# Optimization experiments

Hardware: AMD Instinct MI355X
Metric: run time of the kernel (lower is better)

## Reference

```python
import jax, jax.numpy as jnp
import numpy as np

T, D, H = 1024, 256, 256


def mish(x):
    return x * jnp.tanh(jax.nn.softplus(x))


def layer_norm(x, w, b, eps=1e-5):
    mu = x.mean(-1, keepdims=True)
    var = ((x - mu) ** 2).mean(-1, keepdims=True)
    return (x - mu) / jnp.sqrt(var + eps) * w + b


def setup_inputs() -> dict:
    key = jax.random.key(0)
    ks = jax.random.split(key, 12)
    def glorot(k, sh, fan_in):
        return (jax.random.normal(k, sh, jnp.float32) / np.sqrt(fan_in)).astype(jnp.float32)
    return {
        "x": jax.random.normal(ks[0], (T, D), jnp.float32),
        "s0": jnp.zeros((1, H, H), jnp.float32),
        "z0": jnp.zeros((1, H), jnp.float32),
        "start": jax.random.randint(ks[1], (T + 1,), 0, 2, jnp.int32),
        "done": jax.random.randint(ks[2], (T + 1,), 0, 2, jnp.int32),
        "Wk": glorot(ks[3], (H, D), D),
        "Wq": glorot(ks[4], (H, D), D),
        "Wv": glorot(ks[5], (H, D), D),
        "Wskip": glorot(ks[6], (H, D), D),
        "bskip": jnp.zeros((H,), jnp.float32),
        "W1": glorot(ks[7], (H, H), H),
        "b1": jnp.zeros((H,), jnp.float32),
        "W2": glorot(ks[8], (H, H), H),
        "b2": jnp.zeros((H,), jnp.float32),
        "W3": glorot(ks[9], (H, H), H),
        "b3": jnp.zeros((H,), jnp.float32),
        "ln_w": jnp.ones((H,), jnp.float32),
        "ln_b": jnp.zeros((H,), jnp.float32),
    }


def reference(x, s0, z0, start, done, Wk, Wq, Wv, Wskip, bskip, W1, b1, W2, b2, W3, b3, ln_w, ln_b):
    # feature maps (equinox Linear: y = W @ x, weight is (out,in))
    k = jax.nn.elu(x @ Wk.T)          # [T,H]
    q = jax.nn.elu(x @ Wq.T)          # [T,H]
    v = x @ Wv.T                      # [T,H]
    st = start.astype(x.dtype)[:, None]   # [T+1,1] reset-continuation flags
    dn = done.astype(x.dtype)[:, None]    # [T+1,1]
    # prepend carried state to the sequence, as in the original
    kv = jnp.concatenate([s0, jnp.einsum('ti,tj->tij', k, v)], axis=0)  # [T+1,H,H]
    kk = jnp.concatenate([z0, k], axis=0)                               # [T+1,H]
    def combine(a, b):
        s_a, z_a, _, _ = a
        kv_b, k_b, st_b, dn_b = b
        s = s_a * st_b[..., None] + kv_b * dn_b[..., None]
        z = z_a * st_b + k_b * dn_b
        return (s, z, st_b, dn_b)
    s, z, _, _ = jax.lax.associative_scan(combine, (kv, kk, st, dn))
    # drop the initial-state slot so time indices align with queries
    s_t, z_t = s[1:], z[1:]                          # [T,H,H], [T,H]
    numer = jnp.einsum('ti,tij->tj', q, s_t)         # [T,H]
    denom = jnp.einsum('ti,tj->t', z_t, q).clip(1e-5)  # faithful to source einsum
    out = numer / denom[:, None]
    h = mish(out @ W1.T + b1)
    h = mish(h @ W2.T + b2)
    h = h @ W3.T + b3
    return layer_norm(h + (x @ Wskip.T + bskip), ln_w, ln_b)
```

## Files before the change

kernel.cpp:

```cpp
#include <hip/hip_runtime.h>
#include <math.h>


typedef unsigned long long u64;
typedef unsigned short u16;
typedef __attribute__((ext_vector_type(8))) unsigned short us8;
typedef __attribute__((ext_vector_type(4))) unsigned short us4;
typedef __attribute__((ext_vector_type(8))) short s8;
typedef __attribute__((ext_vector_type(4))) float f4;

__device__ __forceinline__ float eluf(float v) { return v > 0.f ? v : expm1f(v); }
__device__ __forceinline__ float mishf(float v) {
  float sp = fmaxf(v, 0.f) + log1pf(expf(-fabsf(v)));
  return v * tanhf(sp);
}
__device__ __forceinline__ u16 f2bf(float f) {
  unsigned u = __float_as_uint(f);
  unsigned r = u + 0x7FFFu + ((u >> 16) & 1u);
  return (u16)(r >> 16);
}
__device__ __forceinline__ float bf2f(u16 h) { return __uint_as_float((unsigned)h << 16); }

__device__ __forceinline__ f4 mfma16(const u16* a, const u16* b, f4 c) {
  s8 av = *(const s8*)(const void*)a;
  s8 bv = *(const s8*)(const void*)b;
  return __builtin_amdgcn_mfma_f32_16x16x32_bf16(av, bv, c, 0, 0, 0);
}

__device__ __forceinline__ u64 expand32(u64 x) {
  x &= 0xFFFFFFFFull;
  x = (x | (x << 16)) & 0x0000FFFF0000FFFFull;
  x = (x | (x << 8))  & 0x00FF00FF00FF00FFull;
  x = (x | (x << 4))  & 0x0F0F0F0F0F0F0F0Full;
  x = (x | (x << 2))  & 0x3333333333333333ull;
  x = (x | (x << 1))  & 0x5555555555555555ull;
  return x | (x << 1);
}

__device__ __forceinline__ us8 cvt8(const float* p) {
  float4 a = *(const float4*)p;
  float4 b = *(const float4*)(p + 4);
  us8 v;
  v[0] = f2bf(a.x); v[1] = f2bf(a.y); v[2] = f2bf(a.z); v[3] = f2bf(a.w);
  v[4] = f2bf(b.x); v[5] = f2bf(b.y); v[6] = f2bf(b.z); v[7] = f2bf(b.w);
  return v;
}

__global__ __launch_bounds__(256) void qkvs_mask(const float* __restrict__ x,
    const float* __restrict__ Wk, const float* __restrict__ Wq,
    const float* __restrict__ Wv, const float* __restrict__ Wsk,
    const float* __restrict__ bskip,
    const int* __restrict__ start, const int* __restrict__ done,
    u16* __restrict__ Kb, u16* __restrict__ Qb, u16* __restrict__ Vb,
    float* __restrict__ SKP, float* __restrict__ Kpart, u64* __restrict__ Mb) {
  __shared__ u64 SMEM[5810];
  const int tid = threadIdx.x;
  if (blockIdx.x < 256) {
    u16* Xs = (u16*)SMEM;
    u16* Ws = Xs + 2560;
    const int wave = tid >> 6, l = tid & 63;
    const int l15 = l & 15, quad = l >> 4;
    const int rt = blockIdx.x & 15, my = blockIdx.x >> 4;
    const int mat = my >> 2, nt = my & 3;
    const int n0 = nt * 64, mbase = rt * 64;
    const float* Wsrc = (mat == 0) ? Wk : (mat == 1) ? Wq : (mat == 2) ? Wv : Wsk;
    f4 acc[4];
#pragma unroll
    for (int s = 0; s < 4; s++) acc[s] = (f4){0.f, 0.f, 0.f, 0.f};
    const int srow = tid >> 2, sko = (tid & 3) * 8;
    for (int kt = 0; kt < 8; kt++) {
      *(us8*)&Xs[srow * 40 + sko] = cvt8(&x[(mbase + srow) * 256 + kt * 32 + sko]);
      *(us8*)&Ws[srow * 40 + sko] = cvt8(&Wsrc[(n0 + srow) * 256 + kt * 32 + sko]);
      __syncthreads();
      const u16* ap = &Xs[(wave * 16 + l15) * 40 + quad * 8];
#pragma unroll
      for (int s = 0; s < 4; s++)
        acc[s] = mfma16(ap, &Ws[(s * 16 + l15) * 40 + quad * 8], acc[s]);
      __syncthreads();
    }
    const int mw = mbase + wave * 16 + quad * 4;
    if (mat == 0) {
      float tmp[4][4];
#pragma unroll
      for (int s = 0; s < 4; s++)
#pragma unroll
        for (int r = 0; r < 4; r++) {
          float v = eluf(acc[s][r]);
          tmp[s][r] = v;
          Kb[(mw + r) * 256 + n0 + s * 16 + l15] = f2bf(v);
        }
#pragma unroll
      for (int r = 0; r < 4; r++) {
        float t = tmp[0][r] + tmp[1][r] + tmp[2][r] + tmp[3][r];
#pragma unroll
        for (int off = 1; off <= 8; off <<= 1) t += __shfl_xor(t, off);
        if (l15 == 0) Kpart[nt * 1024 + mw + r] = t;
      }
    } else if (mat == 1) {
#pragma unroll
      for (int s = 0; s < 4; s++)
#pragma unroll
        for (int r = 0; r < 4; r++)
          Qb[(mw + r) * 256 + n0 + s * 16 + l15] = f2bf(eluf(acc[s][r]));
    } else if (mat == 2) {
#pragma unroll
      for (int s = 0; s < 4; s++)
#pragma unroll
        for (int r = 0; r < 4; r++)
          Vb[(mw + r) * 256 + n0 + s * 16 + l15] = f2bf(acc[s][r]);
    } else {
#pragma unroll
      for (int s = 0; s < 4; s++) {
        int n = n0 + s * 16 + l15;
        float bv = bskip[n];
#pragma unroll
        for (int r = 0; r < 4; r++)
          SKP[(mw + r) * 256 + n] = acc[s][r] + bv;
      }
    }
    return;
  }
  u64* LV = SMEM;
  unsigned char* sB = (unsigned char*)(SMEM + 5540);
  unsigned char* dB = sB + 1028;
  for (int i = tid; i < 1025; i += 256) {
    sB[i] = (unsigned char)(start[i] != 0);
    dB[i] = (unsigned char)(done[i] != 0);
  }
  if (tid == 0) LV[0] = 1ull;
  __syncthreads();
  const int LOFF[11] = {0, 1407, 383, 127, 63, 31, 15, 7, 3, 1, 0};
  const int GOFF[10] = {5503, 5520, 5528, 5532, 5534, 5535, 5536, 5537, 5538, 5539};
  if (tid < 37) {
    int lv, w;
    if (tid < 17)      { lv = 0; w = tid; }
    else if (tid < 25) { lv = 1; w = tid - 17; }
    else if (tid < 29) { lv = 2; w = tid - 25; }
    else if (tid < 31) { lv = 3; w = tid - 29; }
    else               { lv = tid - 27; w = 0; }
    int n = 1024 >> lv;
    u64 g = 0;
    for (int b = 0; b < 64; b++) {
      int j = (w << 6) + b;
      if (j >= n) break;
      unsigned char bit = (j & 1) ? dB[((j + 1) << lv) - 1] : sB[((j + 2) << lv) - 1];
      g |= (u64)bit << b;
    }
    LV[GOFF[lv] + w] = g;
  }
  __syncthreads();
#pragma unroll
  for (int lv = 9; lv >= 1; lv--) {
    const int n = 1024 >> lv;
    const int nw = (n >= 64) ? (n >> 6) : 1;
    const int nwp = (n >= 128) ? (n >> 7) : 1;
    const int total = n * nw;
    for (int idx = tid; idx < total; idx += 256) {
      int t = idx / nw, w = idx - t * nw;
      u64 word;
      if (t == 0) word = (w == 0) ? 1ull : 0ull;
      else {
        int p = (t & 1) ? (t >> 1) : (t >> 1) - 1;
        u64 pw = LV[LOFF[lv + 1] + p * nwp + (w >> 1)];
        u64 e = expand32((w & 1) ? (pw >> 32) : pw) & LV[GOFF[lv] + w];
        if (t & 1) word = e;
        else {
          int gi = ((t + 1) << lv) - 1;
          word = sB[gi] ? e : 0ull;
          if ((t >> 6) == w) word |= (u64)dB[gi] << (t & 63);
        }
      }
      LV[LOFF[lv] + t * nw + w] = word;
    }
    __syncthreads();
  }
  for (int idx = tid; idx < 1024 * 16; idx += 256) {
    int tp = idx >> 4, wp = idx & 15;
    int t = tp + 1;
    int p = (t & 1) ? (t >> 1) : (t >> 1) - 1;
    u64 sw[2];
#pragma unroll
    for (int u = 0; u < 2; u++) {
      int w = wp + u;
      u64 e = 0;
      if (w < 16) {
        u64 pw = LV[1407 + p * 8 + (w >> 1)];
        e = expand32((w & 1) ? (pw >> 32) : pw) & LV[GOFF[0] + w];
      }
      if (t & 1) sw[u] = e;
      else {
        u64 word = sB[t] ? e : 0ull;
        if ((t >> 6) == w) word |= (u64)dB[t] << (t & 63);
        sw[u] = word;
      }
    }
    Mb[tp * 16 + wp] = (sw[0] >> 1) | (sw[1] << 63);
  }
}

__global__ __launch_bounds__(512) void attn_mlp(
    const u16* __restrict__ Kb, const u16* __restrict__ Qb, const u16* __restrict__ Vb,
    const float* __restrict__ Kpart, const float* __restrict__ SKP,
    const u64* __restrict__ Mb,
    const float* __restrict__ W1, const float* __restrict__ W2, const float* __restrict__ W3,
    const float* __restrict__ b1, const float* __restrict__ b2, const float* __restrict__ b3,
    const float* __restrict__ lnw, const float* __restrict__ lnb,
    float* __restrict__ outp) {
  __shared__ float Ks[1024];
  __shared__ u64 Mw[64];
  __shared__ u16 As[16 * 264];
  __shared__ float Op[8][256];
  __shared__ float dp[8];
  __shared__ u16 WsAll[8 * 640];
  __shared__ float Hbuf[4 * 260];
  const int tid = threadIdx.x, wave = tid >> 6, l = tid & 63;
  const int l15 = l & 15, quad = l >> 4;
  const int m0 = blockIdx.x * 4;
  {
    int j = tid * 2;
    Ks[j] = Kpart[j] + Kpart[1024 + j] + Kpart[2048 + j] + Kpart[3072 + j];
    Ks[j + 1] = Kpart[j + 1] + Kpart[1024 + j + 1] + Kpart[2048 + j + 1] + Kpart[3072 + j + 1];
    if (tid < 64) Mw[tid] = Mb[(m0 + (tid >> 4)) * 16 + (tid & 15)];
  }
  __syncthreads();
  const int r = wave & 3, h = wave >> 2;
  const int tp = m0 + r;
  float q[4], O[4] = {0.f, 0.f, 0.f, 0.f};
  {
    us4 qv = *(const us4*)&Qb[tp * 256 + l * 4];
    q[0] = bf2f(qv.x); q[1] = bf2f(qv.y); q[2] = bf2f(qv.z); q[3] = bf2f(qv.w);
  }
  float qs = q[0] + q[1] + q[2] + q[3];
#pragma unroll
  for (int off = 1; off <= 32; off <<= 1) qs += __shfl_xor(qs, off);
  float d = 0.f;
  for (int w = h * 8; w < h * 8 + 8; w++) {
    u64 bits = Mw[r * 16 + w];
    while (bits) {
      int b = __builtin_ctzll(bits);
      bits &= bits - 1;
      int j = w * 64 + b;
      us4 kv = *(const us4*)&Kb[j * 256 + l * 4];
      us4 vv = *(const us4*)&Vb[j * 256 + l * 4];
      float s = q[0] * bf2f(kv.x) + q[1] * bf2f(kv.y) + q[2] * bf2f(kv.z) + q[3] * bf2f(kv.w);
#pragma unroll
      for (int off = 1; off <= 32; off <<= 1) s += __shfl_xor(s, off);
      d += Ks[j];
      O[0] += s * bf2f(vv.x); O[1] += s * bf2f(vv.y);
      O[2] += s * bf2f(vv.z); O[3] += s * bf2f(vv.w);
    }
  }
#pragma unroll
  for (int i = 0; i < 4; i++) Op[wave][l * 4 + i] = O[i];
  if (l == 0) dp[wave] = d;
  __syncthreads();
  if (h == 0) {
    float dd = dp[r] + dp[r + 4];
    float inv = 1.f / fmaxf(qs * dd, 1e-5f);
    us4 o;
    o.x = f2bf((O[0] + Op[r + 4][l * 4 + 0]) * inv);
    o.y = f2bf((O[1] + Op[r + 4][l * 4 + 1]) * inv);
    o.z = f2bf((O[2] + Op[r + 4][l * 4 + 2]) * inv);
    o.w = f2bf((O[3] + Op[r + 4][l * 4 + 3]) * inv);
    *(us4*)&As[r * 264 + l * 4] = o;
  }
  __syncthreads();
  u16* Wsw = WsAll + wave * 640;
  const int wr = l >> 2, wko = (l & 3) * 8;
#pragma unroll 1
  for (int layer = 0; layer < 3; layer++) {
    const float* Wl = (layer == 0) ? W1 : (layer == 1) ? W2 : W3;
    const float* bias = (layer == 0) ? b1 : (layer == 1) ? b2 : b3;
    f4 acc[2];
#pragma unroll
    for (int c = 0; c < 2; c++) {
      const int nt = wave * 2 + c;
      acc[c] = (f4){0.f, 0.f, 0.f, 0.f};
      for (int kt = 0; kt < 8; kt++) {
        *(us8*)&Wsw[wr * 40 + wko] = cvt8(&Wl[(nt * 16 + wr) * 256 + kt * 32 + wko]);
        const u16* ap = &As[l15 * 264 + kt * 32 + quad * 8];
        acc[c] = mfma16(ap, &Wsw[l15 * 40 + quad * 8], acc[c]);
      }
    }
    __syncthreads();
    if (quad == 0) {
#pragma unroll
      for (int c = 0; c < 2; c++) {
        const int n = (wave * 2 + c) * 16 + l15;
        float bv = bias[n];
        if (layer < 2) {
#pragma unroll
          for (int rr = 0; rr < 4; rr++)
            As[rr * 264 + n] = f2bf(mishf(acc[c][rr] + bv));
        } else {
#pragma unroll
          for (int rr = 0; rr < 4; rr++)
            Hbuf[rr * 260 + n] = acc[c][rr] + bv + SKP[(m0 + rr) * 256 + n];
        }
      }
    }
    __syncthreads();
  }
  if (wave < 4) {
    float hv[4];
#pragma unroll
    for (int i = 0; i < 4; i++) hv[i] = Hbuf[wave * 260 + l * 4 + i];
    float s1 = hv[0] + hv[1] + hv[2] + hv[3];
    float s2 = hv[0] * hv[0] + hv[1] * hv[1] + hv[2] * hv[2] + hv[3] * hv[3];
#pragma unroll
    for (int off = 1; off <= 32; off <<= 1) {
      s1 += __shfl_xor(s1, off);
      s2 += __shfl_xor(s2, off);
    }
    float mu = s1 * (1.f / 256.f);
    float var = s2 * (1.f / 256.f) - mu * mu;
    float rs = rsqrtf(fmaxf(var, 0.f) + 1e-5f);
    float4 wv = *(const float4*)&lnw[l * 4];
    float4 bv = *(const float4*)&lnb[l * 4];
    float4 o;
    o.x = (hv[0] - mu) * rs * wv.x + bv.x;
    o.y = (hv[1] - mu) * rs * wv.y + bv.y;
    o.z = (hv[2] - mu) * rs * wv.z + bv.z;
    o.w = (hv[3] - mu) * rs * wv.w + bv.w;
    *(float4*)&outp[(m0 + wave) * 256 + l * 4] = o;
  }
}

extern "C" void kernel_launch(void* const* d_in, const int* in_sizes, int n_in,
                              void* d_out, int out_size, void* d_ws, size_t ws_size,
                              hipStream_t stream) {
  (void)in_sizes; (void)n_in; (void)out_size; (void)ws_size;
  const float* x   = (const float*)d_in[0];
  const int* start = (const int*)d_in[3];
  const int* done  = (const int*)d_in[4];
  const float* Wk  = (const float*)d_in[5];
  const float* Wq  = (const float*)d_in[6];
  const float* Wv  = (const float*)d_in[7];
  const float* Wsk = (const float*)d_in[8];
  const float* bsk = (const float*)d_in[9];
  const float* W1  = (const float*)d_in[10];
  const float* b1  = (const float*)d_in[11];
  const float* W2  = (const float*)d_in[12];
  const float* b2  = (const float*)d_in[13];
  const float* W3  = (const float*)d_in[14];
  const float* b3  = (const float*)d_in[15];
  const float* lnw = (const float*)d_in[16];
  const float* lnb = (const float*)d_in[17];
  float* out = (float*)d_out;

  char* w = (char*)d_ws;
  u16* Kb      = (u16*)w;
  u16* Qb      = (u16*)(w + 524288);
  u16* Vb      = (u16*)(w + 1048576);
  float* SKP   = (float*)(w + 1572864);
  float* Kpart = (float*)(w + 2621440);
  u64* Mb      = (u64*)(w + 2637824);

  qkvs_mask<<<257, 256, 0, stream>>>(x, Wk, Wq, Wv, Wsk, bsk, start, done,
                                     Kb, Qb, Vb, SKP, Kpart, Mb);
  attn_mlp<<<256, 512, 0, stream>>>(Kb, Qb, Vb, Kpart, SKP, Mb,
                                    W1, W2, W3, b1, b2, b3, lnw, lnb, out);
}
```

Measured before the change: 159.5 us.

## Compute per-block reset mask chain in attention kernel instead of serial mask block

Removes the single serial mask-building block from the projection kernel. Each attention block now rebuilds only the mask path for its own four query rows from start/done flags, using wave ballots for the group words. This takes a long single-block tree over all timesteps off the critical path. In exchange every attention block redoes some flag loading and nine small synchronized levels.

Result: faster. 133.5 us (-16.3%).

```diff
diff --git a/kernel.cpp b/kernel.cpp
--- a/kernel.cpp
+++ b/kernel.cpp
@@ -46,167 +46,87 @@
   return v;
 }
 
-__global__ __launch_bounds__(256) void qkvs_mask(const float* __restrict__ x,
+__global__ __launch_bounds__(256) void qkvs_mfma(const float* __restrict__ x,
     const float* __restrict__ Wk, const float* __restrict__ Wq,
     const float* __restrict__ Wv, const float* __restrict__ Wsk,
     const float* __restrict__ bskip,
-    const int* __restrict__ start, const int* __restrict__ done,
     u16* __restrict__ Kb, u16* __restrict__ Qb, u16* __restrict__ Vb,
-    float* __restrict__ SKP, float* __restrict__ Kpart, u64* __restrict__ Mb) {
-  __shared__ u64 SMEM[5810];
-  const int tid = threadIdx.x;
-  if (blockIdx.x < 256) {
-    u16* Xs = (u16*)SMEM;
-    u16* Ws = Xs + 2560;
-    const int wave = tid >> 6, l = tid & 63;
-    const int l15 = l & 15, quad = l >> 4;
-    const int rt = blockIdx.x & 15, my = blockIdx.x >> 4;
-    const int mat = my >> 2, nt = my & 3;
-    const int n0 = nt * 64, mbase = rt * 64;
-    const float* Wsrc = (mat == 0) ? Wk : (mat == 1) ? Wq : (mat == 2) ? Wv : Wsk;
-    f4 acc[4];
-#pragma unroll
-    for (int s = 0; s < 4; s++) acc[s] = (f4){0.f, 0.f, 0.f, 0.f};
-    const int srow = tid >> 2, sko = (tid & 3) * 8;
-    for (int kt = 0; kt < 8; kt++) {
-      *(us8*)&Xs[srow * 40 + sko] = cvt8(&x[(mbase + srow) * 256 + kt * 32 + sko]);
-      *(us8*)&Ws[srow * 40 + sko] = cvt8(&Wsrc[(n0 + srow) * 256 + kt * 32 + sko]);
-      __syncthreads();
-      const u16* ap = &Xs[(wave * 16 + l15) * 40 + quad * 8];
-#pragma unroll
-      for (int s = 0; s < 4; s++)
-        acc[s] = mfma16(ap, &Ws[(s * 16 + l15) * 40 + quad * 8], acc[s]);
-      __syncthreads();
-    }
-    const int mw = mbase + wave * 16 + quad * 4;
-    if (mat == 0) {
-      float tmp[4][4];
-#pragma unroll
-      for (int s = 0; s < 4; s++)
-#pragma unroll
-        for (int r = 0; r < 4; r++) {
-          float v = eluf(acc[s][r]);
-          tmp[s][r] = v;
-          Kb[(mw + r) * 256 + n0 + s * 16 + l15] = f2bf(v);
-        }
+    float* __restrict__ SKP, float* __restrict__ Kpart) {
+  __shared__ u16 Xs[64 * 40], Ws[64 * 40];
+  const int tid = threadIdx.x, wave = tid >> 6, l = tid & 63;
+  const int l15 = l & 15, quad = l >> 4;
+  const int rt = blockIdx.x & 15, my = blockIdx.x >> 4;
+  const int mat = my >> 2, nt = my & 3;
+  const int n0 = nt * 64, mbase = rt * 64;
+  const float* Wsrc = (mat == 0) ? Wk : (mat == 1) ? Wq : (mat == 2) ? Wv : Wsk;
+  f4 acc[4];
+#pragma unroll
+  for (int s = 0; s < 4; s++) acc[s] = (f4){0.f, 0.f, 0.f, 0.f};
+  const int srow = tid >> 2, sko = (tid & 3) * 8;
+  for (int kt = 0; kt < 8; kt++) {
+    *(us8*)&Xs[srow * 40 + sko] = cvt8(&x[(mbase + srow) * 256 + kt * 32 + sko]);
+    *(us8*)&Ws[srow * 40 + sko] = cvt8(&Wsrc[(n0 + srow) * 256 + kt * 32 + sko]);
+    __syncthreads();
+    const u16* ap = &Xs[(wave * 16 + l15) * 40 + quad * 8];
+#pragma unroll
+    for (int s = 0; s < 4; s++)
+      acc[s] = mfma16(ap, &Ws[(s * 16 + l15) * 40 + quad * 8], acc[s]);
+    __syncthreads();
+  }
+  const int mw = mbase + wave * 16 + quad * 4;
+  if (mat == 0) {
+    float tmp[4][4];
+#pragma unroll
+    for (int s = 0; s < 4; s++)
 #pragma unroll
       for (int r = 0; r < 4; r++) {
-        float t = tmp[0][r] + tmp[1][r] + tmp[2][r] + tmp[3][r];
-#pragma unroll
-        for (int off = 1; off <= 8; off <<= 1) t += __shfl_xor(t, off);
-        if (l15 == 0) Kpart[nt * 1024 + mw + r] = t;
-      }
-    } else if (mat == 1) {
-#pragma unroll
-      for (int s = 0; s < 4; s++)
-#pragma unroll
-        for (int r = 0; r < 4; r++)
-          Qb[(mw + r) * 256 + n0 + s * 16 + l15] = f2bf(eluf(acc[s][r]));
-    } else if (mat == 2) {
-#pragma unroll
-      for (int s = 0; s < 4; s++)
-#pragma unroll
-        for (int r = 0; r < 4; r++)
-          Vb[(mw + r) * 256 + n0 + s * 16 + l15] = f2bf(acc[s][r]);
-    } else {
-#pragma unroll
-      for (int s = 0; s < 4; s++) {
-        int n = n0 + s * 16 + l15;
-        float bv = bskip[n];
-#pragma unroll
-        for (int r = 0; r < 4; r++)
-          SKP[(mw + r) * 256 + n] = acc[s][r] + bv;
-      }
-    }
-    return;
-  }
-  u64* LV = SMEM;
-  unsigned char* sB = (unsigned char*)(SMEM + 5540);
-  unsigned char* dB = sB + 1028;
-  for (int i = tid; i < 1025; i += 256) {
-    sB[i] = (unsigned char)(start[i] != 0);
-    dB[i] = (unsigned char)(done[i] != 0);
-  }
-  if (tid == 0) LV[0] = 1ull;
-  __syncthreads();
-  const int LOFF[11] = {0, 1407, 383, 127, 63, 31, 15, 7, 3, 1, 0};
-  const int GOFF[10] = {5503, 5520, 5528, 5532, 5534, 5535, 5536, 5537, 5538, 5539};
-  if (tid < 37) {
-    int lv, w;
-    if (tid < 17)      { lv = 0; w = tid; }
-    else if (tid < 25) { lv = 1; w = tid - 17; }
-    else if (tid < 29) { lv = 2; w = tid - 25; }
-    else if (tid < 31) { lv = 3; w = tid - 29; }
-    else               { lv = tid - 27; w = 0; }
-    int n = 1024 >> lv;
-    u64 g = 0;
-    for (int b = 0; b < 64; b++) {
-      int j = (w << 6) + b;
-      if (j >= n) break;
-      unsigned char bit = (j & 1) ? dB[((j + 1) << lv) - 1] : sB[((j + 2) << lv) - 1];
-      g |= (u64)bit << b;
-    }
-    LV[GOFF[lv] + w] = g;
-  }
-  __syncthreads();
-#pragma unroll
-  for (int lv = 9; lv >= 1; lv--) {
-    const int n = 1024 >> lv;
-    const int nw = (n >= 64) ? (n >> 6) : 1;
-    const int nwp = (n >= 128) ? (n >> 7) : 1;
-    const int total = n * nw;
-    for (int idx = tid; idx < total; idx += 256) {
-      int t = idx / nw, w = idx - t * nw;
-      u64 word;
-      if (t == 0) word = (w == 0) ? 1ull : 0ull;
-      else {
-        int p = (t & 1) ? (t >> 1) : (t >> 1) - 1;
-        u64 pw = LV[LOFF[lv + 1] + p * nwp + (w >> 1)];
-        u64 e = expand32((w & 1) ? (pw >> 32) : pw) & LV[GOFF[lv] + w];
-        if (t & 1) word = e;
-        else {
-          int gi = ((t + 1) << lv) - 1;
-          word = sB[gi] ? e : 0ull;
-          if ((t >> 6) == w) word |= (u64)dB[gi] << (t & 63);
-        }
-      }
-      LV[LOFF[lv] + t * nw + w] = word;
-    }
-    __syncthreads();
-  }
-  for (int idx = tid; idx < 1024 * 16; idx += 256) {
-    int tp = idx >> 4, wp = idx & 15;
-    int t = tp + 1;
-    int p = (t & 1) ? (t >> 1) : (t >> 1) - 1;
-    u64 sw[2];
-#pragma unroll
-    for (int u = 0; u < 2; u++) {
-      int w = wp + u;
-      u64 e = 0;
-      if (w < 16) {
-        u64 pw = LV[1407 + p * 8 + (w >> 1)];
-        e = expand32((w & 1) ? (pw >> 32) : pw) & LV[GOFF[0] + w];
-      }
-      if (t & 1) sw[u] = e;
-      else {
-        u64 word = sB[t] ? e : 0ull;
-        if ((t >> 6) == w) word |= (u64)dB[t] << (t & 63);
-        sw[u] = word;
-      }
-    }
-    Mb[tp * 16 + wp] = (sw[0] >> 1) | (sw[1] << 63);
+        float v = eluf(acc[s][r]);
+        tmp[s][r] = v;
+        Kb[(mw + r) * 256 + n0 + s * 16 + l15] = f2bf(v);
+      }
+#pragma unroll
+    for (int r = 0; r < 4; r++) {
+      float t = tmp[0][r] + tmp[1][r] + tmp[2][r] + tmp[3][r];
+#pragma unroll
+      for (int off = 1; off <= 8; off <<= 1) t += __shfl_xor(t, off);
+      if (l15 == 0) Kpart[nt * 1024 + mw + r] = t;
+    }
+  } else if (mat == 1) {
+#pragma unroll
+    for (int s = 0; s < 4; s++)
+#pragma unroll
+      for (int r = 0; r < 4; r++)
+        Qb[(mw + r) * 256 + n0 + s * 16 + l15] = f2bf(eluf(acc[s][r]));
+  } else if (mat == 2) {
+#pragma unroll
+    for (int s = 0; s < 4; s++)
+#pragma unroll
+      for (int r = 0; r < 4; r++)
+        Vb[(mw + r) * 256 + n0 + s * 16 + l15] = f2bf(acc[s][r]);
+  } else {
+#pragma unroll
+    for (int s = 0; s < 4; s++) {
+      int n = n0 + s * 16 + l15;
+      float bv = bskip[n];
+#pragma unroll
+      for (int r = 0; r < 4; r++)
+        SKP[(mw + r) * 256 + n] = acc[s][r] + bv;
+    }
   }
 }
 
 __global__ __launch_bounds__(512) void attn_mlp(
     const u16* __restrict__ Kb, const u16* __restrict__ Qb, const u16* __restrict__ Vb,
     const float* __restrict__ Kpart, const float* __restrict__ SKP,
-    const u64* __restrict__ Mb,
+    const int* __restrict__ start, const int* __restrict__ done,
     const float* __restrict__ W1, const float* __restrict__ W2, const float* __restrict__ W3,
     const float* __restrict__ b1, const float* __restrict__ b2, const float* __restrict__ b3,
     const float* __restrict__ lnw, const float* __restrict__ lnb,
     float* __restrict__ outp) {
   __shared__ float Ks[1024];
+  __shared__ unsigned char sBs[1028], dBs[1028];
+  __shared__ u64 GS[37];
+  __shared__ u64 CH[4][21];
   __shared__ u64 Mw[64];
   __shared__ u16 As[16 * 264];
   __shared__ float Op[8][256];
@@ -216,11 +136,80 @@
   const int tid = threadIdx.x, wave = tid >> 6, l = tid & 63;
   const int l15 = l & 15, quad = l >> 4;
   const int m0 = blockIdx.x * 4;
+  for (int i = tid; i < 1025; i += 512) {
+    sBs[i] = (unsigned char)(start[i] != 0);
+    dBs[i] = (unsigned char)(done[i] != 0);
+  }
   {
     int j = tid * 2;
     Ks[j] = Kpart[j] + Kpart[1024 + j] + Kpart[2048 + j] + Kpart[3072 + j];
     Ks[j + 1] = Kpart[j + 1] + Kpart[1024 + j + 1] + Kpart[2048 + j + 1] + Kpart[3072 + j + 1];
-    if (tid < 64) Mw[tid] = Mb[(m0 + (tid >> 4)) * 16 + (tid & 15)];
+  }
+  if (wave < 4 && l == 0) CH[wave][20] = 1ull;
+  __syncthreads();
+  if (wave >= 4) {
+    for (int job = wave - 4; job < 37; job += 4) {
+      int lv, w;
+      if (job < 17)      { lv = 0; w = job; }
+      else if (job < 25) { lv = 1; w = job - 17; }
+      else if (job < 29) { lv = 2; w = job - 25; }
+      else if (job < 31) { lv = 3; w = job - 29; }
+      else               { lv = job - 27; w = 0; }
+      int n = 1024 >> lv;
+      int j = w * 64 + l;
+      int ok = 0;
+      if (j < n)
+        ok = (j & 1) ? dBs[((j + 1) << lv) - 1] : sBs[((j + 2) << lv) - 1];
+      u64 word = __ballot(ok != 0);
+      if (l == 0) GS[(lv == 0) ? w : (lv == 1) ? 17 + w : (lv == 2) ? 25 + w
+                     : (lv == 3) ? 29 + w : 27 + lv] = word;
+    }
+  }
+  __syncthreads();
+  const int CHOFF[11] = {0, 0, 8, 12, 14, 15, 16, 17, 18, 19, 20};
+  const int GOFF2[10] = {0, 17, 25, 29, 31, 32, 33, 34, 35, 36};
+#pragma unroll 1
+  for (int lv = 9; lv >= 1; lv--) {
+    if (wave < 4) {
+      int nw = (1024 >> lv) >= 64 ? ((1024 >> lv) >> 6) : 1;
+      if (l < nw) {
+        int rr = m0 + wave + 1;
+        for (int q = 0; q < lv; q++) rr = (rr & 1) ? (rr >> 1) : (rr >> 1) - 1;
+        u64 word;
+        if (rr <= 0) word = (l == 0 && rr == 0) ? 1ull : 0ull;
+        else {
+          u64 pw = CH[wave][CHOFF[lv + 1] + (l >> 1)];
+          u64 e = expand32((l & 1) ? (pw >> 32) : pw) & GS[GOFF2[lv] + l];
+          if (rr & 1) word = e;
+          else {
+            int gi = ((rr + 1) << lv) - 1;
+            word = sBs[gi] ? e : 0ull;
+            if ((rr >> 6) == l) word |= (u64)dBs[gi] << (rr & 63);
+          }
+        }
+        CH[wave][CHOFF[lv] + l] = word;
+      }
+    }
+    __syncthreads();
+  }
+  if (wave < 4) {
+    const int t = m0 + wave + 1;
+    u64 uw = 0;
+    if (l <= 16) {
+      u64 e = 0;
+      if (l < 16) {
+        u64 pw = CH[wave][(l >> 1)];
+        e = expand32((l & 1) ? (pw >> 32) : pw) & GS[l];
+      }
+      if (t & 1) uw = e;
+      else {
+        uw = sBs[t] ? e : 0ull;
+        if ((t >> 6) == l) uw |= (u64)dBs[t] << (t & 63);
+      }
+    }
+    u64 nxt = __shfl(uw, (l + 1) & 63);
+    u64 mw0 = (uw >> 1) | (nxt << 63);
+    if (l < 16) Mw[wave * 16 + l] = mw0;
   }
   __syncthreads();
   const int r = wave & 3, h = wave >> 2;
@@ -354,10 +343,8 @@
   u16* Vb      = (u16*)(w + 1048576);
   float* SKP   = (float*)(w + 1572864);
   float* Kpart = (float*)(w + 2621440);
-  u64* Mb      = (u64*)(w + 2637824);
-
-  qkvs_mask<<<257, 256, 0, stream>>>(x, Wk, Wq, Wv, Wsk, bsk, start, done,
-                                     Kb, Qb, Vb, SKP, Kpart, Mb);
-  attn_mlp<<<256, 512, 0, stream>>>(Kb, Qb, Vb, Kpart, SKP, Mb,
+
+  qkvs_mfma<<<256, 256, 0, stream>>>(x, Wk, Wq, Wv, Wsk, bsk, Kb, Qb, Vb, SKP, Kpart);
+  attn_mlp<<<256, 512, 0, stream>>>(Kb, Qb, Vb, Kpart, SKP, start, done,
                                     W1, W2, W3, b1, b2, b3, lnw, lnb, out);
 }
```
